# Kernel optimization log

Hardware: AMD Instinct MI355X
Metric: run time of the kernel (lower is better)

Reference implementation:

```python
import jax, jax.numpy as jnp
import numpy as np

IO, H, S, N = 64, 1024, 512, 64

def setup_inputs() -> dict:
    key = jax.random.key(0)
    ks = jax.random.split(key, 6)
    scale = 0.05  # keep activations in a sane range for tanh/softmax
    return {
        "states": jax.random.normal(ks[0], (N, S, H), jnp.float32) * scale,
        "output_set": jax.random.normal(ks[1], (IO, H), jnp.float32) * scale,
        "Wo": jax.random.normal(ks[2], (2 * H, H), jnp.float32) * scale,
        "bo": jax.random.normal(ks[3], (H,), jnp.float32) * scale,
        "Wc": jax.random.normal(ks[4], (IO * H, IO), jnp.float32) * scale,
        "bc": jax.random.normal(ks[5], (IO,), jnp.float32) * scale,
    }

def reference(states, output_set, Wo, bo, Wc, bc):
    # Batched over the n_states Python loop of the original module.
    # attn scores: output_set [io,h] x states [n,s,h] -> [n,io,s]
    attn = jnp.einsum('ih,nsh->nis', output_set, states)
    attn = jax.nn.softmax(attn, axis=-1)  # softmax over context (sm_over_context=True)
    mix = jnp.einsum('nis,nsh->nih', attn, states)            # [n,io,h]
    out = jnp.broadcast_to(output_set[None], mix.shape)       # [n,io,h]
    combined = jnp.concatenate([mix, out], axis=-1)           # [n,io,2h]
    o = combined @ Wo + bo                                    # linear_out: 2h -> h
    logits = jnp.tanh(o).reshape(o.shape[0], -1) @ Wc + bc    # C: io*h -> io
    return logits
```

## Files before the change

### kernel.cpp

```cpp
#include <hip/hip_runtime.h>
#include <hip/hip_bf16.h>

#define IOdim 64
#define Hdim  1024
#define Sdim  512
#define Nbat  64

typedef __bf16 bf16x8_t __attribute__((ext_vector_type(8)));
typedef float  f32x4_t  __attribute__((ext_vector_type(4)));

#define MFMA16(a, b, c) __builtin_amdgcn_mfma_f32_16x16x32_bf16((a), (b), (c), 0, 0, 0)

__device__ __forceinline__ unsigned short f2bf(float f) {
    return __builtin_bit_cast(unsigned short, (__bf16)f);
}
__device__ __forceinline__ bf16x8_t cvt8(float4 p0, float4 p1) {
    bf16x8_t b;
    b[0] = (__bf16)p0.x; b[1] = (__bf16)p0.y; b[2] = (__bf16)p0.z; b[3] = (__bf16)p0.w;
    b[4] = (__bf16)p1.x; b[5] = (__bf16)p1.y; b[6] = (__bf16)p1.z; b[7] = (__bf16)p1.w;
    return b;
}
__device__ __forceinline__ void async16(const void* g, void* l) {
    __builtin_amdgcn_global_load_lds(
        (const __attribute__((address_space(1))) void*)g,
        (__attribute__((address_space(3))) void*)l, 16, 0, 0);
}

__global__ __launch_bounds__(256) void cvt_kernel(const float* __restrict__ in,
                                                  unsigned short* __restrict__ outp,
                                                  int nElem) {
    int idx = blockIdx.x * 256 + threadIdx.x;
    if (idx < nElem) outp[idx] = f2bf(in[idx]);
}

__global__ __launch_bounds__(256) void transpose_cvt(const float* __restrict__ in,
                                                     unsigned short* __restrict__ outp,
                                                     int R, int C) {
    __shared__ float tile[32][33];
    int c0 = blockIdx.x * 32, r0 = blockIdx.y * 32;
    int tx = threadIdx.x, ty = threadIdx.y;
#pragma unroll
    for (int i = 0; i < 4; i++) {
        int r = ty + i * 8;
        tile[r][tx] = in[(size_t)(r0 + r) * C + c0 + tx];
    }
    __syncthreads();
#pragma unroll
    for (int i = 0; i < 4; i++) {
        int r = ty + i * 8;
        outp[(size_t)(c0 + r) * R + r0 + tx] = f2bf(tile[tx][r]);
    }
}

__global__ __launch_bounds__(256) void scores_kernel(const float* __restrict__ states,
                                                     const unsigned short* __restrict__ osb,
                                                     float* __restrict__ attnf) {
    int n = blockIdx.y;
    int tid = threadIdx.x, lane = tid & 63, g = tid >> 6;
    int col = lane & 15, quad = lane >> 4;
    int s = blockIdx.x * 64 + g * 16 + col;
    const float* srow = states + (size_t)(n * Sdim + s) * Hdim + quad * 8;
    const unsigned short* ap = osb + (size_t)col * Hdim + quad * 8;
    f32x4_t acc0 = {0,0,0,0}, acc1 = {0,0,0,0}, acc2 = {0,0,0,0}, acc3 = {0,0,0,0};
    float4 c0 = *(const float4*)(srow);
    float4 c1 = *(const float4*)(srow + 4);
    bf16x8_t A0 = *(const bf16x8_t*)(ap);
    bf16x8_t A1 = *(const bf16x8_t*)(ap + 16 * Hdim);
    bf16x8_t A2 = *(const bf16x8_t*)(ap + 32 * Hdim);
    bf16x8_t A3 = *(const bf16x8_t*)(ap + 48 * Hdim);
#pragma unroll 4
    for (int kc = 0; kc < Hdim - 32; kc += 32) {
        int kn = kc + 32;
        float4 n0 = *(const float4*)(srow + kn);
        float4 n1 = *(const float4*)(srow + kn + 4);
        bf16x8_t N0 = *(const bf16x8_t*)(ap + kn);
        bf16x8_t N1 = *(const bf16x8_t*)(ap + 16 * Hdim + kn);
        bf16x8_t N2 = *(const bf16x8_t*)(ap + 32 * Hdim + kn);
        bf16x8_t N3 = *(const bf16x8_t*)(ap + 48 * Hdim + kn);
        bf16x8_t b = cvt8(c0, c1);
        acc0 = MFMA16(A0, b, acc0);
        acc1 = MFMA16(A1, b, acc1);
        acc2 = MFMA16(A2, b, acc2);
        acc3 = MFMA16(A3, b, acc3);
        c0 = n0; c1 = n1; A0 = N0; A1 = N1; A2 = N2; A3 = N3;
    }
    {
        bf16x8_t b = cvt8(c0, c1);
        acc0 = MFMA16(A0, b, acc0);
        acc1 = MFMA16(A1, b, acc1);
        acc2 = MFMA16(A2, b, acc2);
        acc3 = MFMA16(A3, b, acc3);
    }
    f32x4_t accs[4] = {acc0, acc1, acc2, acc3};
    float* ob = attnf + (size_t)(n * IOdim) * Sdim + blockIdx.x * 64 + g * 16 + col;
#pragma unroll
    for (int ai = 0; ai < 4; ai++)
#pragma unroll
        for (int r = 0; r < 4; r++) {
            int i = ai * 16 + quad * 4 + r;
            ob[i * Sdim] = accs[ai][r];
        }
}

__global__ __launch_bounds__(256) void softmax_kernel(const float* __restrict__ attnf,
                                                      unsigned short* __restrict__ attnb) {
    int row = blockIdx.x * 4 + (threadIdx.x >> 6);
    int lane = threadIdx.x & 63;
    const float* p = attnf + (size_t)row * Sdim + lane * 8;
    float4 v0 = ((const float4*)p)[0];
    float4 v1 = ((const float4*)p)[1];
    float v[8] = {v0.x, v0.y, v0.z, v0.w, v1.x, v1.y, v1.z, v1.w};
    float m = v[0];
#pragma unroll
    for (int j = 1; j < 8; j++) m = fmaxf(m, v[j]);
#pragma unroll
    for (int off = 32; off > 0; off >>= 1) m = fmaxf(m, __shfl_xor(m, off));
    float sum = 0.f;
#pragma unroll
    for (int j = 0; j < 8; j++) { v[j] = __expf(v[j] - m); sum += v[j]; }
#pragma unroll
    for (int off = 32; off > 0; off >>= 1) sum += __shfl_xor(sum, off);
    float inv = 1.0f / sum;
    union { unsigned short u[8]; uint4 q; } res;
#pragma unroll
    for (int j = 0; j < 8; j++) res.u[j] = f2bf(v[j] * inv);
    *(uint4*)(attnb + (size_t)row * Sdim + lane * 8) = res.q;
}

__global__ __launch_bounds__(256) void mix_kernel(const float* __restrict__ states,
                                                  const unsigned short* __restrict__ attnb,
                                                  unsigned short* __restrict__ mixb) {
    __shared__ unsigned short Tlds[64 * 72];
    int n = blockIdx.y, h0 = blockIdx.x * 64;
    int tid = threadIdx.x, lane = tid & 63, g = tid >> 6;
    int col = lane & 15, quad = lane >> 4;
    f32x4_t acc0 = {0,0,0,0}, acc1 = {0,0,0,0}, acc2 = {0,0,0,0}, acc3 = {0,0,0,0};
    const unsigned short* ap = attnb + (size_t)(n * IOdim + col) * Sdim + quad * 8;
    const float* sbase = states + (size_t)n * Sdim * Hdim + h0 + lane;
    float cur[16];
#pragma unroll
    for (int rep = 0; rep < 16; rep++) cur[rep] = sbase[(size_t)(g * 16 + rep) * Hdim];
    for (int sc = 0; sc < Sdim; sc += 64) {
        union { unsigned short u[16]; uint4 q[2]; } pk;
#pragma unroll
        for (int rep = 0; rep < 16; rep++) pk.u[rep] = f2bf(cur[rep]);
        if (sc) __syncthreads();
        *(uint4*)(Tlds + lane * 72 + g * 16)     = pk.q[0];
        *(uint4*)(Tlds + lane * 72 + g * 16 + 8) = pk.q[1];
        if (sc + 64 < Sdim) {
#pragma unroll
            for (int rep = 0; rep < 16; rep++)
                cur[rep] = sbase[(size_t)(sc + 64 + g * 16 + rep) * Hdim];
        }
        __syncthreads();
#pragma unroll
        for (int ks = 0; ks < 64; ks += 32) {
            bf16x8_t b  = *(const bf16x8_t*)(Tlds + (g * 16 + col) * 72 + ks + quad * 8);
            bf16x8_t a0 = *(const bf16x8_t*)(ap + sc + ks);
            bf16x8_t a1 = *(const bf16x8_t*)(ap + 16 * Sdim + sc + ks);
            bf16x8_t a2 = *(const bf16x8_t*)(ap + 32 * Sdim + sc + ks);
            bf16x8_t a3 = *(const bf16x8_t*)(ap + 48 * Sdim + sc + ks);
            acc0 = MFMA16(a0, b, acc0);
            acc1 = MFMA16(a1, b, acc1);
            acc2 = MFMA16(a2, b, acc2);
            acc3 = MFMA16(a3, b, acc3);
        }
    }
    f32x4_t accs[4] = {acc0, acc1, acc2, acc3};
    int h = h0 + g * 16 + col;
#pragma unroll
    for (int ai = 0; ai < 4; ai++)
#pragma unroll
        for (int r = 0; r < 4; r++) {
            int i = ai * 16 + quad * 4 + r;
            mixb[(size_t)(n * IOdim + i) * Hdim + h] = f2bf(accs[ai][r]);
        }
}

__global__ __launch_bounds__(256) void out_gemm(const unsigned short* __restrict__ mixb,
                                                const unsigned short* __restrict__ osb,
                                                const unsigned short* __restrict__ woT,
                                                const float* __restrict__ bo,
                                                unsigned short* __restrict__ tb) {
    __shared__ unsigned short Ald[128 * 32];
    __shared__ unsigned short Bld[128 * 32];
    int h0 = blockIdx.x * 128, r0 = blockIdx.y * 128;
    int tid = threadIdx.x, lane = tid & 63, w = tid >> 6;
    int col = lane & 15, quad = lane >> 4;
    int wx = w & 1, wy = w >> 1;
    int rowA = tid >> 2, seg = tid & 3;
    f32x4_t acc[4][4] = {};
    const unsigned short* m1 = mixb + (size_t)(r0 + rowA) * Hdim + seg * 8;
    const unsigned short* m2 = mixb + (size_t)(r0 + rowA + 64) * Hdim + seg * 8;
    const unsigned short* o1 = osb + (size_t)rowA * Hdim + seg * 8;
    const unsigned short* w1 = woT + (size_t)(h0 + rowA) * 2048 + seg * 8;
    const unsigned short* w2 = woT + (size_t)(h0 + rowA + 64) * 2048 + seg * 8;
    unsigned short* lA1 = Ald + (size_t)tid * 8;
    unsigned short* lA2 = Ald + (size_t)(tid + 256) * 8;
    unsigned short* lB1 = Bld + (size_t)tid * 8;
    unsigned short* lB2 = Bld + (size_t)(tid + 256) * 8;
    for (int kc = 0; kc < 2048; kc += 32) {
        if (kc < 1024) {
            async16(m1 + kc, lA1);
            async16(m2 + kc, lA2);
        } else {
            async16(o1 + (kc - 1024), lA1);
            async16(o1 + (kc - 1024), lA2);
        }
        async16(w1 + kc, lB1);
        async16(w2 + kc, lB2);
        __syncthreads();
        bf16x8_t af[4], bfr[4];
#pragma unroll
        for (int mi = 0; mi < 4; mi++)
            af[mi] = *(const bf16x8_t*)(Ald + (wy * 64 + mi * 16 + col) * 32 + quad * 8);
#pragma unroll
        for (int ni = 0; ni < 4; ni++)
            bfr[ni] = *(const bf16x8_t*)(Bld + (wx * 64 + ni * 16 + col) * 32 + quad * 8);
#pragma unroll
        for (int mi = 0; mi < 4; mi++)
#pragma unroll
            for (int ni = 0; ni < 4; ni++)
                acc[mi][ni] = MFMA16(af[mi], bfr[ni], acc[mi][ni]);
        __syncthreads();
    }
#pragma unroll
    for (int ni = 0; ni < 4; ni++) {
        int h = h0 + wx * 64 + ni * 16 + col;
        float bov = bo[h];
#pragma unroll
        for (int mi = 0; mi < 4; mi++)
#pragma unroll
            for (int r = 0; r < 4; r++) {
                int rr = r0 + wy * 64 + mi * 16 + quad * 4 + r;
                tb[(size_t)rr * Hdim + h] = f2bf(tanhf(acc[mi][ni][r] + bov));
            }
    }
}

__global__ __launch_bounds__(256) void final_gemm(const unsigned short* __restrict__ tb,
                                                  const unsigned short* __restrict__ wcT,
                                                  float* __restrict__ partials) {
    int kc0 = blockIdx.x * 256;
    int tid = threadIdx.x, lane = tid & 63, g = tid >> 6;
    int col = lane & 15, quad = lane >> 4;
    f32x4_t acc0 = {0,0,0,0}, acc1 = {0,0,0,0}, acc2 = {0,0,0,0}, acc3 = {0,0,0,0};
    const unsigned short* ap = tb + (size_t)col * 65536 + kc0 + quad * 8;
    const unsigned short* bp = wcT + (size_t)(g * 16 + col) * 65536 + kc0 + quad * 8;
    bf16x8_t B  = *(const bf16x8_t*)(bp);
    bf16x8_t A0 = *(const bf16x8_t*)(ap);
    bf16x8_t A1 = *(const bf16x8_t*)(ap + (size_t)16 * 65536);
    bf16x8_t A2 = *(const bf16x8_t*)(ap + (size_t)32 * 65536);
    bf16x8_t A3 = *(const bf16x8_t*)(ap + (size_t)48 * 65536);
#pragma unroll
    for (int kc = 0; kc < 256 - 32; kc += 32) {
        int kn = kc + 32;
        bf16x8_t Bn  = *(const bf16x8_t*)(bp + kn);
        bf16x8_t N0 = *(const bf16x8_t*)(ap + kn);
        bf16x8_t N1 = *(const bf16x8_t*)(ap + (size_t)16 * 65536 + kn);
        bf16x8_t N2 = *(const bf16x8_t*)(ap + (size_t)32 * 65536 + kn);
        bf16x8_t N3 = *(const bf16x8_t*)(ap + (size_t)48 * 65536 + kn);
        acc0 = MFMA16(A0, B, acc0);
        acc1 = MFMA16(A1, B, acc1);
        acc2 = MFMA16(A2, B, acc2);
        acc3 = MFMA16(A3, B, acc3);
        B = Bn; A0 = N0; A1 = N1; A2 = N2; A3 = N3;
    }
    acc0 = MFMA16(A0, B, acc0);
    acc1 = MFMA16(A1, B, acc1);
    acc2 = MFMA16(A2, B, acc2);
    acc3 = MFMA16(A3, B, acc3);
    f32x4_t accs[4] = {acc0, acc1, acc2, acc3};
    int j = g * 16 + col;
    float* pb = partials + blockIdx.x * 4096;
#pragma unroll
    for (int ai = 0; ai < 4; ai++)
#pragma unroll
        for (int r = 0; r < 4; r++) {
            int nn = ai * 16 + quad * 4 + r;
            pb[nn * 64 + j] = accs[ai][r];
        }
}

__global__ __launch_bounds__(256) void reduce_kernel(const float* __restrict__ partials,
                                                     const float* __restrict__ bc,
                                                     float* __restrict__ out) {
    int idx = blockIdx.x * 256 + threadIdx.x;
    float s = bc[idx & 63];
#pragma unroll 8
    for (int b = 0; b < 256; b++) s += partials[b * 4096 + idx];
    out[idx] = s;
}

extern "C" void kernel_launch(void* const* d_in, const int* in_sizes, int n_in,
                              void* d_out, int out_size, void* d_ws, size_t ws_size,
                              hipStream_t stream) {
    const float* states     = (const float*)d_in[0];
    const float* output_set = (const float*)d_in[1];
    const float* Wo         = (const float*)d_in[2];
    const float* bo         = (const float*)d_in[3];
    const float* Wc         = (const float*)d_in[4];
    const float* bc         = (const float*)d_in[5];
    float* out = (float*)d_out;

    char* ws = (char*)d_ws;
    float*          attnf = (float*)ws;
    unsigned short* attnb = (unsigned short*)(ws + (8u  << 20));
    unsigned short* mixb  = (unsigned short*)(ws + (12u << 20));
    unsigned short* tb    = (unsigned short*)(ws + (20u << 20));
    unsigned short* woT   = (unsigned short*)(ws + (28u << 20));
    unsigned short* osb   = (unsigned short*)(ws + (32u << 20));
    unsigned short* wcT   = (unsigned short*)(ws + (32u << 20) + (1u << 18));
    float*          parts = (float*)(ws + (41u << 20));

    cvt_kernel<<<dim3(IOdim * Hdim / 256), dim3(256), 0, stream>>>(output_set, osb, IOdim * Hdim);
    transpose_cvt<<<dim3(Hdim / 32, 2048 / 32), dim3(32, 8), 0, stream>>>(Wo, woT, 2048, Hdim);
    transpose_cvt<<<dim3(64 / 32, 65536 / 32), dim3(32, 8), 0, stream>>>(Wc, wcT, 65536, 64);
    scores_kernel<<<dim3(Sdim / 64, Nbat), dim3(256), 0, stream>>>(states, osb, attnf);
    softmax_kernel<<<dim3(Nbat * IOdim / 4), dim3(256), 0, stream>>>(attnf, attnb);
    mix_kernel<<<dim3(Hdim / 64, Nbat), dim3(256), 0, stream>>>(states, attnb, mixb);
    out_gemm<<<dim3(Hdim / 128, Nbat * IOdim / 128), dim3(256), 0, stream>>>(mixb, osb, woT, bo, tb);
    final_gemm<<<dim3(256), dim3(256), 0, stream>>>(tb, wcT, parts);
    reduce_kernel<<<dim3(16), dim3(256), 0, stream>>>(parts, bc, out);
}
```

Baseline: 344.5 us.

## Split scores, out_gemm and final_gemm across more blocks with double-buffered prefetch

The scores kernel now gives each block 32 context positions and each wave a 16x32 sub-tile with two-deep register prefetch. out_gemm narrows its output tile from 128 to 64 columns, and final_gemm splits K into 128-wide chunks across 512 blocks. Together these double the grid sizes to raise occupancy and latency hiding on the many CUs. The cost is more redundant operand loads per output, and the reduce kernel must now sum twice as many partials. The partials buffer reuses the attnf workspace region.

```diff
diff --git a/kernel.cpp b/kernel.cpp
--- a/kernel.cpp
+++ b/kernel.cpp
@@ -56,49 +56,44 @@
                                                      const unsigned short* __restrict__ osb,
                                                      float* __restrict__ attnf) {
     int n = blockIdx.y;
-    int tid = threadIdx.x, lane = tid & 63, g = tid >> 6;
+    int tid = threadIdx.x, lane = tid & 63, w = tid >> 6;
     int col = lane & 15, quad = lane >> 4;
-    int s = blockIdx.x * 64 + g * 16 + col;
+    int sh = w & 1, ih = w >> 1;
+    int s = blockIdx.x * 32 + sh * 16 + col;
     const float* srow = states + (size_t)(n * Sdim + s) * Hdim + quad * 8;
-    const unsigned short* ap = osb + (size_t)col * Hdim + quad * 8;
-    f32x4_t acc0 = {0,0,0,0}, acc1 = {0,0,0,0}, acc2 = {0,0,0,0}, acc3 = {0,0,0,0};
-    float4 c0 = *(const float4*)(srow);
-    float4 c1 = *(const float4*)(srow + 4);
-    bf16x8_t A0 = *(const bf16x8_t*)(ap);
-    bf16x8_t A1 = *(const bf16x8_t*)(ap + 16 * Hdim);
-    bf16x8_t A2 = *(const bf16x8_t*)(ap + 32 * Hdim);
-    bf16x8_t A3 = *(const bf16x8_t*)(ap + 48 * Hdim);
+    const unsigned short* ap = osb + (size_t)(ih * 32 + col) * Hdim + quad * 8;
+    f32x4_t acc0 = {0,0,0,0}, acc1 = {0,0,0,0};
+    float4 pc0[2], pc1[2];
+    bf16x8_t pA0[2], pA1[2];
+#pragma unroll
+    for (int t = 0; t < 2; t++) {
+        pc0[t] = *(const float4*)(srow + t * 32);
+        pc1[t] = *(const float4*)(srow + t * 32 + 4);
+        pA0[t] = *(const bf16x8_t*)(ap + t * 32);
+        pA1[t] = *(const bf16x8_t*)(ap + 16 * Hdim + t * 32);
+    }
 #pragma unroll 4
-    for (int kc = 0; kc < Hdim - 32; kc += 32) {
-        int kn = kc + 32;
-        float4 n0 = *(const float4*)(srow + kn);
-        float4 n1 = *(const float4*)(srow + kn + 4);
-        bf16x8_t N0 = *(const bf16x8_t*)(ap + kn);
-        bf16x8_t N1 = *(const bf16x8_t*)(ap + 16 * Hdim + kn);
-        bf16x8_t N2 = *(const bf16x8_t*)(ap + 32 * Hdim + kn);
-        bf16x8_t N3 = *(const bf16x8_t*)(ap + 48 * Hdim + kn);
-        bf16x8_t b = cvt8(c0, c1);
-        acc0 = MFMA16(A0, b, acc0);
-        acc1 = MFMA16(A1, b, acc1);
-        acc2 = MFMA16(A2, b, acc2);
-        acc3 = MFMA16(A3, b, acc3);
-        c0 = n0; c1 = n1; A0 = N0; A1 = N1; A2 = N2; A3 = N3;
-    }
-    {
-        bf16x8_t b = cvt8(c0, c1);
-        acc0 = MFMA16(A0, b, acc0);
-        acc1 = MFMA16(A1, b, acc1);
-        acc2 = MFMA16(A2, b, acc2);
-        acc3 = MFMA16(A3, b, acc3);
-    }
-    f32x4_t accs[4] = {acc0, acc1, acc2, acc3};
-    float* ob = attnf + (size_t)(n * IOdim) * Sdim + blockIdx.x * 64 + g * 16 + col;
-#pragma unroll
-    for (int ai = 0; ai < 4; ai++)
+    for (int kc = 0; kc < Hdim; kc += 32) {
+        int p = (kc >> 5) & 1;
+        bf16x8_t b = cvt8(pc0[p], pc1[p]);
+        acc0 = MFMA16(pA0[p], b, acc0);
+        acc1 = MFMA16(pA1[p], b, acc1);
+        int kn = kc + 64;
+        if (kn < Hdim) {
+            pc0[p] = *(const float4*)(srow + kn);
+            pc1[p] = *(const float4*)(srow + kn + 4);
+            pA0[p] = *(const bf16x8_t*)(ap + kn);
+            pA1[p] = *(const bf16x8_t*)(ap + 16 * Hdim + kn);
+        }
+    }
+    f32x4_t accs[2] = {acc0, acc1};
+    float* ob = attnf + (size_t)(n * IOdim) * Sdim + blockIdx.x * 32 + sh * 16 + col;
+#pragma unroll
+    for (int t = 0; t < 2; t++)
 #pragma unroll
         for (int r = 0; r < 4; r++) {
-            int i = ai * 16 + quad * 4 + r;
-            ob[i * Sdim] = accs[ai][r];
+            int i = ih * 32 + t * 16 + quad * 4 + r;
+            ob[i * Sdim] = accs[t][r];
         }
 }
 
@@ -183,50 +178,48 @@
                                                 const float* __restrict__ bo,
                                                 unsigned short* __restrict__ tb) {
     __shared__ unsigned short Ald[128 * 32];
-    __shared__ unsigned short Bld[128 * 32];
-    int h0 = blockIdx.x * 128, r0 = blockIdx.y * 128;
+    __shared__ unsigned short Bld[64 * 32];
+    int h0 = blockIdx.x * 64, r0 = blockIdx.y * 128;
     int tid = threadIdx.x, lane = tid & 63, w = tid >> 6;
     int col = lane & 15, quad = lane >> 4;
     int wx = w & 1, wy = w >> 1;
-    int rowA = tid >> 2, seg = tid & 3;
-    f32x4_t acc[4][4] = {};
-    const unsigned short* m1 = mixb + (size_t)(r0 + rowA) * Hdim + seg * 8;
-    const unsigned short* m2 = mixb + (size_t)(r0 + rowA + 64) * Hdim + seg * 8;
-    const unsigned short* o1 = osb + (size_t)rowA * Hdim + seg * 8;
-    const unsigned short* w1 = woT + (size_t)(h0 + rowA) * 2048 + seg * 8;
-    const unsigned short* w2 = woT + (size_t)(h0 + rowA + 64) * 2048 + seg * 8;
+    int rowX = tid >> 2, seg = tid & 3;
+    f32x4_t acc[4][2] = {};
+    const unsigned short* m1 = mixb + (size_t)(r0 + rowX) * Hdim + seg * 8;
+    const unsigned short* m2 = mixb + (size_t)(r0 + rowX + 64) * Hdim + seg * 8;
+    const unsigned short* o1 = osb + (size_t)rowX * Hdim + seg * 8;
+    const unsigned short* w1 = woT + (size_t)(h0 + rowX) * 2048 + seg * 8;
     unsigned short* lA1 = Ald + (size_t)tid * 8;
     unsigned short* lA2 = Ald + (size_t)(tid + 256) * 8;
     unsigned short* lB1 = Bld + (size_t)tid * 8;
-    unsigned short* lB2 = Bld + (size_t)(tid + 256) * 8;
     for (int kc = 0; kc < 2048; kc += 32) {
         if (kc < 1024) {
             async16(m1 + kc, lA1);
             async16(m2 + kc, lA2);
         } else {
-            async16(o1 + (kc - 1024), lA1);
-            async16(o1 + (kc - 1024), lA2);
+            int k2 = kc - 1024;
+            async16(o1 + k2, lA1);
+            async16(o1 + k2, lA2);
         }
         async16(w1 + kc, lB1);
-        async16(w2 + kc, lB2);
         __syncthreads();
-        bf16x8_t af[4], bfr[4];
+        bf16x8_t af[4], bfr[2];
 #pragma unroll
         for (int mi = 0; mi < 4; mi++)
             af[mi] = *(const bf16x8_t*)(Ald + (wy * 64 + mi * 16 + col) * 32 + quad * 8);
 #pragma unroll
-        for (int ni = 0; ni < 4; ni++)
-            bfr[ni] = *(const bf16x8_t*)(Bld + (wx * 64 + ni * 16 + col) * 32 + quad * 8);
+        for (int ni = 0; ni < 2; ni++)
+            bfr[ni] = *(const bf16x8_t*)(Bld + (wx * 32 + ni * 16 + col) * 32 + quad * 8);
 #pragma unroll
         for (int mi = 0; mi < 4; mi++)
 #pragma unroll
-            for (int ni = 0; ni < 4; ni++)
+            for (int ni = 0; ni < 2; ni++)
                 acc[mi][ni] = MFMA16(af[mi], bfr[ni], acc[mi][ni]);
         __syncthreads();
     }
 #pragma unroll
-    for (int ni = 0; ni < 4; ni++) {
-        int h = h0 + wx * 64 + ni * 16 + col;
+    for (int ni = 0; ni < 2; ni++) {
+        int h = h0 + wx * 32 + ni * 16 + col;
         float bov = bo[h];
 #pragma unroll
         for (int mi = 0; mi < 4; mi++)
@@ -241,35 +234,37 @@
 __global__ __launch_bounds__(256) void final_gemm(const unsigned short* __restrict__ tb,
                                                   const unsigned short* __restrict__ wcT,
                                                   float* __restrict__ partials) {
-    int kc0 = blockIdx.x * 256;
+    int kc0 = blockIdx.x * 128;
     int tid = threadIdx.x, lane = tid & 63, g = tid >> 6;
     int col = lane & 15, quad = lane >> 4;
     f32x4_t acc0 = {0,0,0,0}, acc1 = {0,0,0,0}, acc2 = {0,0,0,0}, acc3 = {0,0,0,0};
     const unsigned short* ap = tb + (size_t)col * 65536 + kc0 + quad * 8;
     const unsigned short* bp = wcT + (size_t)(g * 16 + col) * 65536 + kc0 + quad * 8;
-    bf16x8_t B  = *(const bf16x8_t*)(bp);
-    bf16x8_t A0 = *(const bf16x8_t*)(ap);
-    bf16x8_t A1 = *(const bf16x8_t*)(ap + (size_t)16 * 65536);
-    bf16x8_t A2 = *(const bf16x8_t*)(ap + (size_t)32 * 65536);
-    bf16x8_t A3 = *(const bf16x8_t*)(ap + (size_t)48 * 65536);
-#pragma unroll
-    for (int kc = 0; kc < 256 - 32; kc += 32) {
-        int kn = kc + 32;
-        bf16x8_t Bn  = *(const bf16x8_t*)(bp + kn);
-        bf16x8_t N0 = *(const bf16x8_t*)(ap + kn);
-        bf16x8_t N1 = *(const bf16x8_t*)(ap + (size_t)16 * 65536 + kn);
-        bf16x8_t N2 = *(const bf16x8_t*)(ap + (size_t)32 * 65536 + kn);
-        bf16x8_t N3 = *(const bf16x8_t*)(ap + (size_t)48 * 65536 + kn);
-        acc0 = MFMA16(A0, B, acc0);
-        acc1 = MFMA16(A1, B, acc1);
-        acc2 = MFMA16(A2, B, acc2);
-        acc3 = MFMA16(A3, B, acc3);
-        B = Bn; A0 = N0; A1 = N1; A2 = N2; A3 = N3;
-    }
-    acc0 = MFMA16(A0, B, acc0);
-    acc1 = MFMA16(A1, B, acc1);
-    acc2 = MFMA16(A2, B, acc2);
-    acc3 = MFMA16(A3, B, acc3);
+    bf16x8_t B[2], A0[2], A1[2], A2[2], A3[2];
+#pragma unroll
+    for (int t = 0; t < 2; t++) {
+        B[t]  = *(const bf16x8_t*)(bp + t * 32);
+        A0[t] = *(const bf16x8_t*)(ap + t * 32);
+        A1[t] = *(const bf16x8_t*)(ap + (size_t)16 * 65536 + t * 32);
+        A2[t] = *(const bf16x8_t*)(ap + (size_t)32 * 65536 + t * 32);
+        A3[t] = *(const bf16x8_t*)(ap + (size_t)48 * 65536 + t * 32);
+    }
+#pragma unroll
+    for (int c = 0; c < 4; c++) {
+        int p = c & 1;
+        acc0 = MFMA16(A0[p], B[p], acc0);
+        acc1 = MFMA16(A1[p], B[p], acc1);
+        acc2 = MFMA16(A2[p], B[p], acc2);
+        acc3 = MFMA16(A3[p], B[p], acc3);
+        if (c + 2 < 4) {
+            int kn = (c + 2) * 32;
+            B[p]  = *(const bf16x8_t*)(bp + kn);
+            A0[p] = *(const bf16x8_t*)(ap + kn);
+            A1[p] = *(const bf16x8_t*)(ap + (size_t)16 * 65536 + kn);
+            A2[p] = *(const bf16x8_t*)(ap + (size_t)32 * 65536 + kn);
+            A3[p] = *(const bf16x8_t*)(ap + (size_t)48 * 65536 + kn);
+        }
+    }
     f32x4_t accs[4] = {acc0, acc1, acc2, acc3};
     int j = g * 16 + col;
     float* pb = partials + blockIdx.x * 4096;
@@ -288,7 +283,7 @@
     int idx = blockIdx.x * 256 + threadIdx.x;
     float s = bc[idx & 63];
 #pragma unroll 8
-    for (int b = 0; b < 256; b++) s += partials[b * 4096 + idx];
+    for (int b = 0; b < 512; b++) s += partials[b * 4096 + idx];
     out[idx] = s;
 }
 
@@ -305,21 +300,21 @@
 
     char* ws = (char*)d_ws;
     float*          attnf = (float*)ws;
+    float*          parts = (float*)ws;
     unsigned short* attnb = (unsigned short*)(ws + (8u  << 20));
     unsigned short* mixb  = (unsigned short*)(ws + (12u << 20));
     unsigned short* tb    = (unsigned short*)(ws + (20u << 20));
     unsigned short* woT   = (unsigned short*)(ws + (28u << 20));
     unsigned short* osb   = (unsigned short*)(ws + (32u << 20));
     unsigned short* wcT   = (unsigned short*)(ws + (32u << 20) + (1u << 18));
-    float*          parts = (float*)(ws + (41u << 20));
 
     cvt_kernel<<<dim3(IOdim * Hdim / 256), dim3(256), 0, stream>>>(output_set, osb, IOdim * Hdim);
     transpose_cvt<<<dim3(Hdim / 32, 2048 / 32), dim3(32, 8), 0, stream>>>(Wo, woT, 2048, Hdim);
     transpose_cvt<<<dim3(64 / 32, 65536 / 32), dim3(32, 8), 0, stream>>>(Wc, wcT, 65536, 64);
-    scores_kernel<<<dim3(Sdim / 64, Nbat), dim3(256), 0, stream>>>(states, osb, attnf);
+    scores_kernel<<<dim3(Sdim / 32, Nbat), dim3(256), 0, stream>>>(states, osb, attnf);
     softmax_kernel<<<dim3(Nbat * IOdim / 4), dim3(256), 0, stream>>>(attnf, attnb);
     mix_kernel<<<dim3(Hdim / 64, Nbat), dim3(256), 0, stream>>>(states, attnb, mixb);
-    out_gemm<<<dim3(Hdim / 128, Nbat * IOdim / 128), dim3(256), 0, stream>>>(mixb, osb, woT, bo, tb);
-    final_gemm<<<dim3(256), dim3(256), 0, stream>>>(tb, wcT, parts);
+    out_gemm<<<dim3(Hdim / 64, Nbat * IOdim / 128), dim3(256), 0, stream>>>(mixb, osb, woT, bo, tb);
+    final_gemm<<<dim3(512), dim3(256), 0, stream>>>(tb, wcT, parts);
     reduce_kernel<<<dim3(16), dim3(256), 0, stream>>>(parts, bc, out);
 }
```

Measured after the change: 355.2 us. 3.1% more time.
